# Kernel tuning notes

Hardware: AMD Instinct MI355X
Metric: run time of the kernel (lower is better)

The kernel has to match this reference:

```python
import jax, jax.numpy as jnp
import numpy as np

T = 2048          # tokens
HID = 4096        # hidden_size
H = 32            # n_heads
D = 192           # head_dim
DR = 64           # qk_rope_head_dim
Q_LORA = 1536
O_LORA = 512
G = 4             # o_groups
EPS = 1e-6
MAX_POS = 4096
ROPE_BASE = 10000.0
SCALE = D ** -0.5


def _rmsnorm(x, weight=None, eps=EPS):
    # normalize over last dim in fp32, like the triton kernel / RMSNorm
    xf = x.astype(jnp.float32)
    rms_inv = jax.lax.rsqrt(jnp.mean(xf * xf, axis=-1, keepdims=True) + eps)
    out = xf * rms_inv
    if weight is not None:
        out = out * weight
    return out.astype(x.dtype)


def _apply_rope(x, cos, sin):
    # x: [..., DR]; interleaved complex rotation (deepseek-style freqs_cis mult)
    x2 = x.reshape(x.shape[:-1] + (DR // 2, 2))
    a, b = x2[..., 0], x2[..., 1]
    ra = a * cos - b * sin
    rb = a * sin + b * cos
    return jnp.stack([ra, rb], axis=-1).reshape(x.shape)


def setup_inputs() -> dict:
    key = jax.random.key(0)
    ks = jax.random.split(key, 12)
    s = lambda k, shape, scale: jax.random.normal(k, shape, dtype=jnp.float32) * scale
    x = s(ks[0], (T, HID), 1.0)
    positions = jnp.arange(T, dtype=jnp.int64)
    wq_a = s(ks[1], (Q_LORA, HID), HID ** -0.5)
    q_norm_w = jnp.ones((Q_LORA,), jnp.float32)
    wq_b = s(ks[2], (H * D, Q_LORA), Q_LORA ** -0.5)
    wkv = s(ks[3], (D, HID), HID ** -0.5)
    kv_norm_w = jnp.ones((D,), jnp.float32)
    attn_sink = s(ks[4], (H,), 1.0)
    wo_a = s(ks[5], (G * O_LORA, (H * D) // G), ((H * D) // G) ** -0.5)
    wo_b = s(ks[6], (HID, G * O_LORA), (G * O_LORA) ** -0.5)
    # precomputed rope tables [MAX_POS, DR//2]
    inv_freq = 1.0 / (ROPE_BASE ** (np.arange(0, DR, 2, dtype=np.float32) / DR))
    t = np.arange(MAX_POS, dtype=np.float32)
    freqs = np.outer(t, inv_freq)
    rope_cos = jnp.asarray(np.cos(freqs))
    rope_sin = jnp.asarray(np.sin(freqs))
    return dict(x=x, positions=positions, wq_a=wq_a, q_norm_w=q_norm_w, wq_b=wq_b,
                wkv=wkv, kv_norm_w=kv_norm_w, attn_sink=attn_sink, wo_a=wo_a,
                wo_b=wo_b, rope_cos=rope_cos, rope_sin=rope_sin)


def reference(x, positions, wq_a, q_norm_w, wq_b, wkv, kv_norm_w, attn_sink,
              wo_a, wo_b, rope_cos, rope_sin):
    cos = rope_cos[positions]  # [T, DR//2]
    sin = rope_sin[positions]

    # q path: wq_a -> RMSNorm(weighted) -> wq_b -> per-head unweighted RMSNorm -> RoPE
    q_lora = _rmsnorm(x @ wq_a.T, q_norm_w)                # [T, Q_LORA]
    q = (q_lora @ wq_b.T).reshape(T, H, D)                 # [T, H, D]
    q = _rmsnorm(q)                                        # per-head rms_normalize
    q_rope = _apply_rope(q[..., -DR:], cos[:, None, :], sin[:, None, :])
    q = jnp.concatenate([q[..., :-DR], q_rope], axis=-1)

    # shared single kv head: wkv -> kv_norm -> RoPE on rope dims
    kv = _rmsnorm(x @ wkv.T, kv_norm_w)                    # [T, D]
    kv_rope = _apply_rope(kv[..., -DR:], cos, sin)
    kv = jnp.concatenate([kv[..., :-DR], kv_rope], axis=-1)

    # MQA attention with attention sink and causal mask
    scores = jnp.einsum('thd,sd->ths', q, kv).astype(jnp.float32) * SCALE  # [T,H,S]
    causal = positions[:, None] >= positions[None, :]       # [T, S]
    scores = jnp.where(causal[:, None, :], scores, -jnp.inf)
    sink = jnp.broadcast_to(attn_sink[None, :, None], (T, H, 1))
    logits = jnp.concatenate([scores, sink], axis=-1)       # [T, H, S+1]
    probs = jax.nn.softmax(logits, axis=-1)[..., :-1]       # drop sink column
    out = jnp.einsum('ths,sd->thd', probs.astype(kv.dtype), kv)  # [T, H, D]

    # grouped low-rank output projection: wo_a per group, then wo_b
    out_g = out.reshape(T, G, (H * D) // G)
    wo_a_g = wo_a.reshape(G, O_LORA, (H * D) // G)
    o_low = jnp.einsum('tgi,goi->tgo', out_g, wo_a_g).reshape(T, G * O_LORA)
    y = o_low @ wo_b.T                                      # [T, HID]
    return y
```

## Files before the change

### kernel.cpp

```cpp
#include <hip/hip_runtime.h>
#include <hip/hip_bf16.h>

#define T_TOK 2048
#define HIDN  4096
#define NH    32
#define HD    192
#define QLORA 1536
#define OLORA 512
#define NG    4
#define NFUSE 1728

typedef unsigned short u16;
typedef __attribute__((ext_vector_type(8))) short short8;
typedef __attribute__((ext_vector_type(4))) short short4v;
typedef __attribute__((ext_vector_type(4))) float f32x4;

__device__ __forceinline__ float b2f(u16 u) {
  union { unsigned int u; float f; } x; x.u = ((unsigned int)u) << 16; return x.f;
}
__device__ __forceinline__ u16 f2b(float f) {
  union { float f; unsigned int u; } x; x.f = f;
  unsigned int r = x.u + 0x7fff + ((x.u >> 16) & 1);
  return (u16)(r >> 16);
}

#define GLOAD16(gp, lp) __builtin_amdgcn_global_load_lds( \
    (const __attribute__((address_space(1))) unsigned int*)(gp), \
    (__attribute__((address_space(3))) unsigned int*)(lp), 16, 0, 0)
#define SCHEDB() __builtin_amdgcn_sched_barrier(0)
#define SBAR()   __builtin_amdgcn_s_barrier()

__global__ __launch_bounds__(256) void cast_f32_bf16(const float* __restrict__ src,
                                                     u16* __restrict__ dst, long n4) {
  long i = (long)blockIdx.x * blockDim.x + threadIdx.x;
  long stride = (long)gridDim.x * blockDim.x;
  for (long j = i; j < n4; j += stride) {
    float4 v = *reinterpret_cast<const float4*>(src + j * 4);
    short4v o;
    o[0] = (short)f2b(v.x); o[1] = (short)f2b(v.y);
    o[2] = (short)f2b(v.z); o[3] = (short)f2b(v.w);
    *reinterpret_cast<short4v*>(dst + j * 4) = o;
  }
}

template <int OM>
__global__ __launch_bounds__(256)
void gemm_bt(const u16* __restrict__ A, const u16* __restrict__ B,
             void* __restrict__ Cout, int M, int N, int K,
             int lda, int ldb, int ldc,
             long a_goff, long b_goff, long c_goff) {
  A += (long)blockIdx.z * a_goff;
  B += (long)blockIdx.z * b_goff;
  __shared__ u16 As[2][128 * 32];
  __shared__ u16 Bs[2][128 * 32];
  const int tid = threadIdx.x;
  const int lane = tid & 63;
  const int wave = tid >> 6;
  const int lg = lane >> 4, lr = lane & 15;
  const int wm = (wave >> 1) * 64, wn = (wave & 1) * 64;
  const int m0 = blockIdx.x * 128, n0 = blockIdx.y * 128;

  const int i0 = tid, i1 = tid + 256;
  const int ra0 = i0 >> 2, ka0 = (i0 & 3) * 8;
  const int ra1 = i1 >> 2, ka1 = (i1 & 3) * 8;
  const u16* pA0 = A + (long)(m0 + ra0) * lda + ka0;
  const u16* pA1 = A + (long)(m0 + ra1) * lda + ka1;
  int rb0 = n0 + ra0; if (rb0 > N - 1) rb0 = N - 1;
  int rb1 = n0 + ra1; if (rb1 > N - 1) rb1 = N - 1;
  const u16* pB0 = B + (long)rb0 * ldb + ka0;
  const u16* pB1 = B + (long)rb1 * ldb + ka1;
  const int woff = wave * 1024;

  f32x4 acc[4][4];
#pragma unroll
  for (int a = 0; a < 4; a++)
#pragma unroll
    for (int b = 0; b < 4; b++) acc[a][b] = f32x4{0.f, 0.f, 0.f, 0.f};

  GLOAD16(pA0, (char*)As + woff);
  GLOAD16(pA1, (char*)As + 4096 + woff);
  GLOAD16(pB0, (char*)Bs + woff);
  GLOAD16(pB1, (char*)Bs + 4096 + woff);

  const int nk = K >> 5;
  int buf = 0;
  for (int kk = 0; kk < nk; ++kk) {
    const int kn = (kk + 1 < nk) ? (kk + 1) * 32 : kk * 32;
    {
      char* dA = (char*)As + (buf ^ 1) * 8192 + woff;
      char* dB = (char*)Bs + (buf ^ 1) * 8192 + woff;
      GLOAD16(pA0 + kn, dA);
      GLOAD16(pA1 + kn, dA + 4096);
      GLOAD16(pB0 + kn, dB);
      GLOAD16(pB1 + kn, dB + 4096);
    }
    asm volatile("s_waitcnt vmcnt(4)" ::: "memory");
    SCHEDB(); SBAR(); SCHEDB();

    short8 af[4], bf[4];
#pragma unroll
    for (int i = 0; i < 4; i++)
      af[i] = *reinterpret_cast<const short8*>(&As[buf][(wm + i * 16 + lr) * 32 + lg * 8]);
#pragma unroll
    for (int i = 0; i < 4; i++)
      bf[i] = *reinterpret_cast<const short8*>(&Bs[buf][(wn + i * 16 + lr) * 32 + lg * 8]);
#pragma unroll
    for (int mi = 0; mi < 4; mi++)
#pragma unroll
      for (int ni = 0; ni < 4; ni++)
        acc[mi][ni] = __builtin_amdgcn_mfma_f32_16x16x32_bf16(af[mi], bf[ni], acc[mi][ni], 0, 0, 0);

    SCHEDB(); SBAR(); SCHEDB();
    buf ^= 1;
  }
  asm volatile("s_waitcnt vmcnt(0)" ::: "memory");

  const long cbase = (long)blockIdx.z * c_goff;
#pragma unroll
  for (int mi = 0; mi < 4; mi++) {
#pragma unroll
    for (int ni = 0; ni < 4; ni++) {
      int col = n0 + wn + ni * 16 + lr;
      if (col < N) {
#pragma unroll
        for (int i = 0; i < 4; i++) {
          int row = m0 + wm + mi * 16 + lg * 4 + i;
          float v = acc[mi][ni][i];
          if constexpr (OM == 0)
            reinterpret_cast<u16*>(Cout)[cbase + (long)row * ldc + col] = f2b(v);
          else
            reinterpret_cast<float*>(Cout)[cbase + (long)row * ldc + col] = v;
        }
      }
    }
  }
}

__global__ __launch_bounds__(256)
void rmsnorm_rows(u16* __restrict__ buf, const float* __restrict__ w) {
  const int row = blockIdx.x;
  u16* p = buf + (long)row * NFUSE;
  const int tid = threadIdx.x;
  float v[6];
  float ss = 0.f;
#pragma unroll
  for (int j = 0; j < 6; j++) { v[j] = b2f(p[tid + j * 256]); ss += v[j] * v[j]; }
#pragma unroll
  for (int m = 1; m < 64; m <<= 1) ss += __shfl_xor(ss, m);
  __shared__ float red[4];
  if ((tid & 63) == 0) red[tid >> 6] = ss;
  __syncthreads();
  ss = red[0] + red[1] + red[2] + red[3];
  float rinv = rsqrtf(ss * (1.0f / QLORA) + 1e-6f);
#pragma unroll
  for (int j = 0; j < 6; j++) p[tid + j * 256] = f2b(v[j] * rinv * w[tid + j * 256]);
}

__global__ __launch_bounds__(256)
void qnorm_rope(u16* __restrict__ q, const int* __restrict__ pos,
                const float* __restrict__ rc, const float* __restrict__ rs) {
  const int t = blockIdx.x, h = blockIdx.y * 4 + (threadIdx.x >> 6);
  u16* p = q + (long)t * (NH * HD) + h * HD;
  const int lane = threadIdx.x & 63;
  float v0 = b2f(p[lane]), v1 = b2f(p[lane + 64]), v2 = b2f(p[lane + 128]);
  float ss = v0 * v0 + v1 * v1 + v2 * v2;
#pragma unroll
  for (int m = 1; m < 64; m <<= 1) ss += __shfl_xor(ss, m);
  float rinv = rsqrtf(ss * (1.0f / HD) + 1e-6f);
  v0 *= rinv; v1 *= rinv; v2 *= rinv;
  float partner = __shfl_xor(v2, 1);
  int pp = pos[t];
  int j = lane >> 1;
  float c = rc[pp * 32 + j], s = rs[pp * 32 + j];
  float r = ((lane & 1) == 0) ? (v2 * c - partner * s) : (partner * s + v2 * c);
  p[lane] = f2b(v0); p[lane + 64] = f2b(v1); p[lane + 128] = f2b(r);
}

__global__ __launch_bounds__(256)
void kvnorm_rope(const u16* __restrict__ t1f, u16* __restrict__ kvb,
                 u16* __restrict__ kvT, const float* __restrict__ w,
                 const int* __restrict__ pos,
                 const float* __restrict__ rc, const float* __restrict__ rs) {
  const int t = blockIdx.x * 4 + (threadIdx.x >> 6);
  const u16* src = t1f + (long)t * NFUSE + QLORA;
  u16* p = kvb + (long)t * HD;
  const int lane = threadIdx.x & 63;
  float v0 = b2f(src[lane]), v1 = b2f(src[lane + 64]), v2 = b2f(src[lane + 128]);
  float ss = v0 * v0 + v1 * v1 + v2 * v2;
#pragma unroll
  for (int m = 1; m < 64; m <<= 1) ss += __shfl_xor(ss, m);
  float rinv = rsqrtf(ss * (1.0f / HD) + 1e-6f);
  v0 *= rinv * w[lane]; v1 *= rinv * w[lane + 64]; v2 *= rinv * w[lane + 128];
  float partner = __shfl_xor(v2, 1);
  int pp = pos[t];
  int j = lane >> 1;
  float c = rc[pp * 32 + j], s = rs[pp * 32 + j];
  float r = ((lane & 1) == 0) ? (v2 * c - partner * s) : (partner * s + v2 * c);
  u16 o0 = f2b(v0), o1 = f2b(v1), o2 = f2b(r);
  p[lane] = o0; p[lane + 64] = o1; p[lane + 128] = o2;
  kvT[(long)lane * T_TOK + t] = o0;
  kvT[(long)(lane + 64) * T_TOK + t] = o1;
  kvT[(long)(lane + 128) * T_TOK + t] = o2;
}

__global__ __launch_bounds__(512)
void attn(const u16* __restrict__ q, const u16* __restrict__ kv,
          const u16* __restrict__ kvT, const float* __restrict__ sink,
          u16* __restrict__ out) {
  __shared__ u16 Ks[2][64 * 192];
  __shared__ u16 Vs[2][192 * 64];
  __shared__ u16 P[8][16 * 68];
  const int tid = threadIdx.x;
  const int wave = tid >> 6, lane = tid & 63;
  const int lg = lane >> 4, lr = lane & 15;
  const int h = blockIdx.y * 8 + wave;
  u16* Pw = P[wave];

  int krow[3], koff[3], vrow[3], voff[3];
#pragma unroll
  for (int j = 0; j < 3; j++) {
    int s = tid + j * 512;
    int rk = s / 24, ck = s - rk * 24;
    krow[j] = rk; koff[j] = (ck ^ (rk & 7)) * 8;
    int rv = s >> 3, cv = s & 7;
    vrow[j] = rv; voff[j] = (cv ^ (rv & 7)) * 8;
  }
  const float sk = sink[h];
  const float scale = 0.07216878364870323f;
  int buf = 0;

  for (int pass = 0; pass < 2; ++pass) {
    const int qb = pass ? blockIdx.x : (127 - blockIdx.x);
    const int q0 = qb * 16;
    const int s_end = q0 + 16;
    const int nt = (s_end + 63) >> 6;

    short8 qf[6];
#pragma unroll
    for (int c = 0; c < 6; c++)
      qf[c] = *reinterpret_cast<const short8*>(
          q + (long)(q0 + lr) * (NH * HD) + h * HD + c * 32 + lg * 8);

    f32x4 acc[12];
#pragma unroll
    for (int c = 0; c < 12; c++) acc[c] = f32x4{0.f, 0.f, 0.f, 0.f};
    float mr[4], lrow[4];
#pragma unroll
    for (int i = 0; i < 4; i++) { mr[i] = sk; lrow[i] = 1.0f; }

    {
      char* dK = (char*)Ks[buf]; char* dV = (char*)Vs[buf];
#pragma unroll
      for (int j = 0; j < 3; j++)
        GLOAD16(kv + (long)krow[j] * HD + koff[j], dK + (tid + j * 512) * 16);
#pragma unroll
      for (int j = 0; j < 3; j++)
        GLOAD16(kvT + (long)vrow[j] * T_TOK + voff[j], dV + (tid + j * 512) * 16);
    }

    for (int t = 0; t < nt; ++t) {
      const int s0 = t * 64;
      const int sn = (t + 1 < nt) ? s0 + 64 : s0;
      {
        char* dK = (char*)Ks[buf ^ 1]; char* dV = (char*)Vs[buf ^ 1];
#pragma unroll
        for (int j = 0; j < 3; j++)
          GLOAD16(kv + (long)(sn + krow[j]) * HD + koff[j], dK + (tid + j * 512) * 16);
#pragma unroll
        for (int j = 0; j < 3; j++)
          GLOAD16(kvT + (long)vrow[j] * T_TOK + sn + voff[j], dV + (tid + j * 512) * 16);
      }
      asm volatile("s_waitcnt vmcnt(6)" ::: "memory");
      SCHEDB(); SBAR(); SCHEDB();

      const u16* Kb = Ks[buf];
      const u16* Vb = Vs[buf];
      f32x4 sc[4];
      __builtin_amdgcn_s_setprio(1);
#pragma unroll
      for (int sub = 0; sub < 4; sub++) {
        int c0 = s0 + sub * 16;
        f32x4 v = f32x4{0.f, 0.f, 0.f, 0.f};
        if (c0 < s_end) {
#pragma unroll
          for (int c = 0; c < 6; c++) {
            short8 kf = *reinterpret_cast<const short8*>(
                &Kb[((sub * 16 + lr) * HD + c * 32 + lg * 8) ^ ((lr & 7) << 3)]);
            v = __builtin_amdgcn_mfma_f32_16x16x32_bf16(qf[c], kf, v, 0, 0, 0);
          }
          int scol = c0 + lr;
#pragma unroll
          for (int i = 0; i < 4; i++) {
            int qrow = q0 + lg * 4 + i;
            v[i] = (scol <= qrow) ? v[i] * scale : -__builtin_inff();
          }
        } else {
#pragma unroll
          for (int i = 0; i < 4; i++) v[i] = -__builtin_inff();
        }
        sc[sub] = v;
      }
      __builtin_amdgcn_s_setprio(0);

      float mn[4];
#pragma unroll
      for (int i = 0; i < 4; i++) {
        float tm = fmaxf(fmaxf(sc[0][i], sc[1][i]), fmaxf(sc[2][i], sc[3][i]));
#pragma unroll
        for (int m = 1; m < 16; m <<= 1) tm = fmaxf(tm, __shfl_xor(tm, m));
        mn[i] = fmaxf(mr[i], tm);
      }
      bool need = (mn[0] > mr[0]) | (mn[1] > mr[1]) | (mn[2] > mr[2]) | (mn[3] > mr[3]);
      if (__any(need)) {
#pragma unroll
        for (int i = 0; i < 4; i++) {
          float f = __expf(mr[i] - mn[i]);
          lrow[i] *= f; mr[i] = mn[i];
#pragma unroll
          for (int c = 0; c < 12; c++) acc[c][i] *= f;
        }
      }
      float pr[4][4];
#pragma unroll
      for (int i = 0; i < 4; i++) {
        float rsum = 0.f;
#pragma unroll
        for (int sub = 0; sub < 4; sub++) { pr[sub][i] = __expf(sc[sub][i] - mr[i]); rsum += pr[sub][i]; }
#pragma unroll
        for (int m = 1; m < 16; m <<= 1) rsum += __shfl_xor(rsum, m);
        lrow[i] += rsum;
      }
#pragma unroll
      for (int sub = 0; sub < 4; sub++)
#pragma unroll
        for (int i = 0; i < 4; i++)
          Pw[(lg * 4 + i) * 68 + sub * 16 + lr] = f2b(pr[sub][i]);
      short8 pf0 = *reinterpret_cast<const short8*>(&Pw[lr * 68 + lg * 8]);
      short8 pf1 = *reinterpret_cast<const short8*>(&Pw[lr * 68 + 32 + lg * 8]);

      __builtin_amdgcn_s_setprio(1);
#pragma unroll
      for (int c = 0; c < 12; c++) {
        short8 vf = *reinterpret_cast<const short8*>(
            &Vb[((c * 16 + lr) * 64 + lg * 8) ^ ((lr & 7) << 3)]);
        acc[c] = __builtin_amdgcn_mfma_f32_16x16x32_bf16(pf0, vf, acc[c], 0, 0, 0);
      }
      if (s0 + 32 < s_end) {
#pragma unroll
        for (int c = 0; c < 12; c++) {
          short8 vf = *reinterpret_cast<const short8*>(
              &Vb[((c * 16 + lr) * 64 + 32 + lg * 8) ^ ((lr & 7) << 3)]);
          acc[c] = __builtin_amdgcn_mfma_f32_16x16x32_bf16(pf1, vf, acc[c], 0, 0, 0);
        }
      }
      __builtin_amdgcn_s_setprio(0);

      SCHEDB(); SBAR(); SCHEDB();
      buf ^= 1;
    }

    asm volatile("s_waitcnt vmcnt(0)" ::: "memory");
#pragma unroll
    for (int c = 0; c < 12; c++)
#pragma unroll
      for (int i = 0; i < 4; i++) {
        int qrow = q0 + lg * 4 + i;
        out[(long)qrow * (NH * HD) + h * HD + c * 16 + lr] = f2b(acc[c][i] / lrow[i]);
      }
    SBAR();
  }
}

extern "C" void kernel_launch(void* const* d_in, const int* in_sizes, int n_in,
                              void* d_out, int out_size, void* d_ws, size_t ws_size,
                              hipStream_t stream) {
  const float* x    = (const float*)d_in[0];
  const int* pos    = (const int*)d_in[1];
  const float* wq_a = (const float*)d_in[2];
  const float* q_nw = (const float*)d_in[3];
  const float* wq_b = (const float*)d_in[4];
  const float* wkv  = (const float*)d_in[5];
  const float* kvnw = (const float*)d_in[6];
  const float* sink = (const float*)d_in[7];
  const float* wo_a = (const float*)d_in[8];
  const float* wo_b = (const float*)d_in[9];
  const float* rcos = (const float*)d_in[10];
  const float* rsin = (const float*)d_in[11];
  float* y = (float*)d_out;

  char* ws = (char*)d_ws;
  size_t off = 0;
  auto alloc = [&](size_t bytes) -> void* {
    void* p = ws + off;
    off += (bytes + 255) & ~(size_t)255;
    return p;
  };
  u16* xb   = (u16*)alloc((size_t)T_TOK * HIDN * 2);
  u16* wqab = (u16*)alloc((size_t)QLORA * HIDN * 2);
  u16* wkvb = (u16*)alloc((size_t)HD * HIDN * 2);
  u16* wqbb = (u16*)alloc((size_t)NH * HD * QLORA * 2);
  u16* woab = (u16*)alloc((size_t)NG * OLORA * 1536 * 2);
  u16* wobb = (u16*)alloc((size_t)HIDN * NG * OLORA * 2);
  u16* t1f  = (u16*)alloc((size_t)T_TOK * NFUSE * 2);
  u16* qn   = (u16*)alloc((size_t)T_TOK * NH * HD * 2);
  u16* kvb  = (u16*)alloc((size_t)T_TOK * HD * 2);
  u16* kvT  = (u16*)alloc((size_t)HD * T_TOK * 2);
  u16* ao   = (u16*)alloc((size_t)T_TOK * NH * HD * 2);
  u16* olow = (u16*)alloc((size_t)T_TOK * NG * OLORA * 2);

  auto cast = [&](const float* s, u16* d, long n) {
    long n4 = n / 4;
    long blocks = (n4 + 255) / 256;
    if (blocks > 2048) blocks = 2048;
    hipLaunchKernelGGL(cast_f32_bf16, dim3((int)blocks), dim3(256), 0, stream, s, d, n4);
  };
  cast(x, xb, (long)T_TOK * HIDN);
  cast(wq_a, wqab, (long)QLORA * HIDN);
  cast(wkv, wkvb, (long)HD * HIDN);
  cast(wq_b, wqbb, (long)NH * HD * QLORA);
  cast(wo_a, woab, (long)NG * OLORA * 1536);
  cast(wo_b, wobb, (long)HIDN * NG * OLORA);

  hipLaunchKernelGGL((gemm_bt<0>), dim3(16, 14, 1), dim3(256), 0, stream,
                     xb, wqab, (void*)t1f, 2048, NFUSE, 4096, 4096, 4096, NFUSE, 0L, 0L, 0L);
  hipLaunchKernelGGL(rmsnorm_rows, dim3(2048), dim3(256), 0, stream, t1f, q_nw);
  hipLaunchKernelGGL(kvnorm_rope, dim3(512), dim3(256), 0, stream,
                     t1f, kvb, kvT, kvnw, pos, rcos, rsin);
  hipLaunchKernelGGL((gemm_bt<0>), dim3(16, 48, 1), dim3(256), 0, stream,
                     t1f, wqbb, (void*)qn, 2048, 6144, 1536, NFUSE, 1536, 6144, 0L, 0L, 0L);
  hipLaunchKernelGGL(qnorm_rope, dim3(2048, 8), dim3(256), 0, stream, qn, pos, rcos, rsin);
  hipLaunchKernelGGL(attn, dim3(64, 4), dim3(512), 0, stream, qn, kvb, kvT, sink, ao);
  hipLaunchKernelGGL((gemm_bt<0>), dim3(16, 4, 4), dim3(256), 0, stream,
                     ao, woab, (void*)olow, 2048, 512, 1536, 6144, 1536, 2048,
                     1536L, (long)512 * 1536, 512L);
  hipLaunchKernelGGL((gemm_bt<1>), dim3(16, 32, 1), dim3(256), 0, stream,
                     olow, wobb, (void*)y, 2048, 4096, 2048, 2048, 2048, 4096, 0L, 0L, 0L);
}
```

Baseline: 410.3 us.

## Run both causal passes concurrently in 1024-thread attention blocks, fuse casts, fold scale

The attention kernel now launches 16 waves per block: half handle the long (reversed) query tile and half the short tile, sharing one K/V staging pipeline instead of doing two sequential passes. The softmax scale and log2(e) are folded into Q during qnorm_rope so the kernel can use exp2f and skip the per-score multiply. The six f32->bf16 cast launches are merged into a single kernel. In exchange, the short-tile waves sit idle once their causal range is done, and 1024-thread blocks limit occupancy and register budget.

```diff
diff --git a/kernel.cpp b/kernel.cpp
--- a/kernel.cpp
+++ b/kernel.cpp
@@ -30,17 +30,30 @@
 #define SCHEDB() __builtin_amdgcn_sched_barrier(0)
 #define SBAR()   __builtin_amdgcn_s_barrier()
 
-__global__ __launch_bounds__(256) void cast_f32_bf16(const float* __restrict__ src,
-                                                     u16* __restrict__ dst, long n4) {
-  long i = (long)blockIdx.x * blockDim.x + threadIdx.x;
-  long stride = (long)gridDim.x * blockDim.x;
-  for (long j = i; j < n4; j += stride) {
+__device__ __forceinline__ void cast_seg(const float* __restrict__ src,
+                                         u16* __restrict__ dst, long n4,
+                                         long idx, long stride) {
+  for (long j = idx; j < n4; j += stride) {
     float4 v = *reinterpret_cast<const float4*>(src + j * 4);
     short4v o;
     o[0] = (short)f2b(v.x); o[1] = (short)f2b(v.y);
     o[2] = (short)f2b(v.z); o[3] = (short)f2b(v.w);
     *reinterpret_cast<short4v*>(dst + j * 4) = o;
   }
+}
+
+__global__ __launch_bounds__(256)
+void cast6(const float* s0, u16* d0, long n0, const float* s1, u16* d1, long n1,
+           const float* s2, u16* d2, long n2, const float* s3, u16* d3, long n3,
+           const float* s4, u16* d4, long n4c, const float* s5, u16* d5, long n5) {
+  long idx = (long)blockIdx.x * blockDim.x + threadIdx.x;
+  long stride = (long)gridDim.x * blockDim.x;
+  cast_seg(s0, d0, n0, idx, stride);
+  cast_seg(s1, d1, n1, idx, stride);
+  cast_seg(s2, d2, n2, idx, stride);
+  cast_seg(s3, d3, n3, idx, stride);
+  cast_seg(s4, d4, n4c, idx, stride);
+  cast_seg(s5, d5, n5, idx, stride);
 }
 
 template <int OM>
@@ -162,6 +175,7 @@
   const int t = blockIdx.x, h = blockIdx.y * 4 + (threadIdx.x >> 6);
   u16* p = q + (long)t * (NH * HD) + h * HD;
   const int lane = threadIdx.x & 63;
+  const float QS = 0.07216878364870323f * 1.4426950408889634f;
   float v0 = b2f(p[lane]), v1 = b2f(p[lane + 64]), v2 = b2f(p[lane + 128]);
   float ss = v0 * v0 + v1 * v1 + v2 * v2;
 #pragma unroll
@@ -173,7 +187,7 @@
   int j = lane >> 1;
   float c = rc[pp * 32 + j], s = rs[pp * 32 + j];
   float r = ((lane & 1) == 0) ? (v2 * c - partner * s) : (partner * s + v2 * c);
-  p[lane] = f2b(v0); p[lane + 64] = f2b(v1); p[lane + 128] = f2b(r);
+  p[lane] = f2b(v0 * QS); p[lane + 64] = f2b(v1 * QS); p[lane + 128] = f2b(r * QS);
 }
 
 __global__ __launch_bounds__(256)
@@ -203,76 +217,74 @@
   kvT[(long)(lane + 128) * T_TOK + t] = o2;
 }
 
-__global__ __launch_bounds__(512)
+__global__ __launch_bounds__(1024, 4)
 void attn(const u16* __restrict__ q, const u16* __restrict__ kv,
           const u16* __restrict__ kvT, const float* __restrict__ sink,
           u16* __restrict__ out) {
   __shared__ u16 Ks[2][64 * 192];
   __shared__ u16 Vs[2][192 * 64];
-  __shared__ u16 P[8][16 * 68];
+  __shared__ u16 P[16][16 * 68];
   const int tid = threadIdx.x;
   const int wave = tid >> 6, lane = tid & 63;
   const int lg = lane >> 4, lr = lane & 15;
-  const int h = blockIdx.y * 8 + wave;
+  const int role = wave >> 3;
+  const int h = blockIdx.y * 8 + (wave & 7);
+  const int bx = blockIdx.x;
+  const int q0 = role ? bx * 16 : (127 - bx) * 16;
+  const int s_end = q0 + 16;
+  const int ntL = ((127 - bx) * 16 + 16 + 63) >> 6;
   u16* Pw = P[wave];
 
-  int krow[3], koff[3], vrow[3], voff[3];
+  int srow[3], soff[3], sdst[3], skind[3];
 #pragma unroll
   for (int j = 0; j < 3; j++) {
-    int s = tid + j * 512;
-    int rk = s / 24, ck = s - rk * 24;
-    krow[j] = rk; koff[j] = (ck ^ (rk & 7)) * 8;
-    int rv = s >> 3, cv = s & 7;
-    vrow[j] = rv; voff[j] = (cv ^ (rv & 7)) * 8;
+    int g = j * 1024 + tid;
+    if (g < 1536) {
+      int rk = g / 24, ck = g - rk * 24;
+      srow[j] = rk; soff[j] = (ck ^ (rk & 7)) * 8; sdst[j] = g * 16; skind[j] = 1;
+    } else {
+      int vc = g - 1536;
+      int rv = vc >> 3, cv = vc & 7;
+      srow[j] = rv; soff[j] = (cv ^ (rv & 7)) * 8; sdst[j] = vc * 16; skind[j] = 0;
+    }
   }
-  const float sk = sink[h];
-  const float scale = 0.07216878364870323f;
+
+#define STAGE(BUF, S0) do { \
+    _Pragma("unroll") \
+    for (int j = 0; j < 3; j++) { \
+      if (skind[j]) \
+        GLOAD16(kv + (long)((S0) + srow[j]) * HD + soff[j], (char*)Ks[BUF] + sdst[j]); \
+      else \
+        GLOAD16(kvT + (long)srow[j] * T_TOK + (S0) + soff[j], (char*)Vs[BUF] + sdst[j]); \
+    } \
+  } while (0)
+
+  const float sk = sink[h] * 1.4426950408889634f;
+
+  short8 qf[6];
+#pragma unroll
+  for (int c = 0; c < 6; c++)
+    qf[c] = *reinterpret_cast<const short8*>(
+        q + (long)(q0 + lr) * (NH * HD) + h * HD + c * 32 + lg * 8);
+
+  f32x4 acc[12];
+#pragma unroll
+  for (int c = 0; c < 12; c++) acc[c] = f32x4{0.f, 0.f, 0.f, 0.f};
+  float mr[4], lrow[4];
+#pragma unroll
+  for (int i = 0; i < 4; i++) { mr[i] = sk; lrow[i] = 1.0f; }
+
+  STAGE(0, 0);
+
   int buf = 0;
-
-  for (int pass = 0; pass < 2; ++pass) {
-    const int qb = pass ? blockIdx.x : (127 - blockIdx.x);
-    const int q0 = qb * 16;
-    const int s_end = q0 + 16;
-    const int nt = (s_end + 63) >> 6;
-
-    short8 qf[6];
-#pragma unroll
-    for (int c = 0; c < 6; c++)
-      qf[c] = *reinterpret_cast<const short8*>(
-          q + (long)(q0 + lr) * (NH * HD) + h * HD + c * 32 + lg * 8);
-
-    f32x4 acc[12];
-#pragma unroll
-    for (int c = 0; c < 12; c++) acc[c] = f32x4{0.f, 0.f, 0.f, 0.f};
-    float mr[4], lrow[4];
-#pragma unroll
-    for (int i = 0; i < 4; i++) { mr[i] = sk; lrow[i] = 1.0f; }
-
-    {
-      char* dK = (char*)Ks[buf]; char* dV = (char*)Vs[buf];
-#pragma unroll
-      for (int j = 0; j < 3; j++)
-        GLOAD16(kv + (long)krow[j] * HD + koff[j], dK + (tid + j * 512) * 16);
-#pragma unroll
-      for (int j = 0; j < 3; j++)
-        GLOAD16(kvT + (long)vrow[j] * T_TOK + voff[j], dV + (tid + j * 512) * 16);
-    }
-
-    for (int t = 0; t < nt; ++t) {
-      const int s0 = t * 64;
-      const int sn = (t + 1 < nt) ? s0 + 64 : s0;
-      {
-        char* dK = (char*)Ks[buf ^ 1]; char* dV = (char*)Vs[buf ^ 1];
-#pragma unroll
-        for (int j = 0; j < 3; j++)
-          GLOAD16(kv + (long)(sn + krow[j]) * HD + koff[j], dK + (tid + j * 512) * 16);
-#pragma unroll
-        for (int j = 0; j < 3; j++)
-          GLOAD16(kvT + (long)vrow[j] * T_TOK + sn + voff[j], dV + (tid + j * 512) * 16);
-      }
-      asm volatile("s_waitcnt vmcnt(6)" ::: "memory");
-      SCHEDB(); SBAR(); SCHEDB();
-
+  for (int t = 0; t < ntL; ++t) {
+    const int s0 = t * 64;
+    const int sn = (t + 1 < ntL) ? s0 + 64 : s0;
+    STAGE(buf ^ 1, sn);
+    asm volatile("s_waitcnt vmcnt(3)" ::: "memory");
+    SCHEDB(); SBAR(); SCHEDB();
+
+    if (s0 < s_end) {
       const u16* Kb = Ks[buf];
       const u16* Vb = Vs[buf];
       f32x4 sc[4];
@@ -292,7 +304,7 @@
 #pragma unroll
           for (int i = 0; i < 4; i++) {
             int qrow = q0 + lg * 4 + i;
-            v[i] = (scol <= qrow) ? v[i] * scale : -__builtin_inff();
+            v[i] = (scol <= qrow) ? v[i] : -__builtin_inff();
           }
         } else {
 #pragma unroll
@@ -314,7 +326,7 @@
       if (__any(need)) {
 #pragma unroll
         for (int i = 0; i < 4; i++) {
-          float f = __expf(mr[i] - mn[i]);
+          float f = exp2f(mr[i] - mn[i]);
           lrow[i] *= f; mr[i] = mn[i];
 #pragma unroll
           for (int c = 0; c < 12; c++) acc[c][i] *= f;
@@ -325,7 +337,7 @@
       for (int i = 0; i < 4; i++) {
         float rsum = 0.f;
 #pragma unroll
-        for (int sub = 0; sub < 4; sub++) { pr[sub][i] = __expf(sc[sub][i] - mr[i]); rsum += pr[sub][i]; }
+        for (int sub = 0; sub < 4; sub++) { pr[sub][i] = exp2f(sc[sub][i] - mr[i]); rsum += pr[sub][i]; }
 #pragma unroll
         for (int m = 1; m < 16; m <<= 1) rsum += __shfl_xor(rsum, m);
         lrow[i] += rsum;
@@ -354,21 +366,21 @@
         }
       }
       __builtin_amdgcn_s_setprio(0);
-
-      SCHEDB(); SBAR(); SCHEDB();
-      buf ^= 1;
     }
 
-    asm volatile("s_waitcnt vmcnt(0)" ::: "memory");
-#pragma unroll
-    for (int c = 0; c < 12; c++)
-#pragma unroll
-      for (int i = 0; i < 4; i++) {
-        int qrow = q0 + lg * 4 + i;
-        out[(long)qrow * (NH * HD) + h * HD + c * 16 + lr] = f2b(acc[c][i] / lrow[i]);
-      }
-    SBAR();
+    SCHEDB(); SBAR(); SCHEDB();
+    buf ^= 1;
   }
+  asm volatile("s_waitcnt vmcnt(0)" ::: "memory");
+
+#pragma unroll
+  for (int c = 0; c < 12; c++)
+#pragma unroll
+    for (int i = 0; i < 4; i++) {
+      int qrow = q0 + lg * 4 + i;
+      out[(long)qrow * (NH * HD) + h * HD + c * 16 + lr] = f2b(acc[c][i] / lrow[i]);
+    }
+#undef STAGE
 }
 
 extern "C" void kernel_launch(void* const* d_in, const int* in_sizes, int n_in,
@@ -408,18 +420,13 @@
   u16* ao   = (u16*)alloc((size_t)T_TOK * NH * HD * 2);
   u16* olow = (u16*)alloc((size_t)T_TOK * NG * OLORA * 2);
 
-  auto cast = [&](const float* s, u16* d, long n) {
-    long n4 = n / 4;
-    long blocks = (n4 + 255) / 256;
-    if (blocks > 2048) blocks = 2048;
-    hipLaunchKernelGGL(cast_f32_bf16, dim3((int)blocks), dim3(256), 0, stream, s, d, n4);
-  };
-  cast(x, xb, (long)T_TOK * HIDN);
-  cast(wq_a, wqab, (long)QLORA * HIDN);
-  cast(wkv, wkvb, (long)HD * HIDN);
-  cast(wq_b, wqbb, (long)NH * HD * QLORA);
-  cast(wo_a, woab, (long)NG * OLORA * 1536);
-  cast(wo_b, wobb, (long)HIDN * NG * OLORA);
+  hipLaunchKernelGGL(cast6, dim3(1024), dim3(256), 0, stream,
+                     x,    xb,   (long)T_TOK * HIDN / 4,
+                     wq_a, wqab, (long)QLORA * HIDN / 4,
+                     wkv,  wkvb, (long)HD * HIDN / 4,
+                     wq_b, wqbb, (long)NH * HD * QLORA / 4,
+                     wo_a, woab, (long)NG * OLORA * 1536 / 4,
+                     wo_b, wobb, (long)HIDN * NG * OLORA / 4);
 
   hipLaunchKernelGGL((gemm_bt<0>), dim3(16, 14, 1), dim3(256), 0, stream,
                      xb, wqab, (void*)t1f, 2048, NFUSE, 4096, 4096, 4096, NFUSE, 0L, 0L, 0L);
@@ -429,7 +436,7 @@
   hipLaunchKernelGGL((gemm_bt<0>), dim3(16, 48, 1), dim3(256), 0, stream,
                      t1f, wqbb, (void*)qn, 2048, 6144, 1536, NFUSE, 1536, 6144, 0L, 0L, 0L);
   hipLaunchKernelGGL(qnorm_rope, dim3(2048, 8), dim3(256), 0, stream, qn, pos, rcos, rsin);
-  hipLaunchKernelGGL(attn, dim3(64, 4), dim3(512), 0, stream, qn, kvb, kvT, sink, ao);
+  hipLaunchKernelGGL(attn, dim3(64, 4), dim3(1024), 0, stream, qn, kvb, kvT, sink, ao);
   hipLaunchKernelGGL((gemm_bt<0>), dim3(16, 4, 4), dim3(256), 0, stream,
                      ao, woab, (void*)olow, 2048, 512, 1536, 6144, 1536, 2048,
                      1536L, (long)512 * 1536, 512L);
```

After: 723.3 us. 1.76x slower.

## Fuse weight casts, swizzle GEMM block order, fold softmax scale into q

Applied to the files above, without the earlier changes.

The six fp32-to-bf16 cast launches become a single grid-stride kernel. GEMM blocks are remapped with an XCD-style swizzle (groups of 8) to improve L2 locality across chiplets. The attention scale and log2(e) are folded into q during the norm/rope pass so the softmax can use exp2 without a per-score multiply; this rounds the scaled q to bf16, which slightly changes numerics.

```diff
diff --git a/kernel.cpp b/kernel.cpp
--- a/kernel.cpp
+++ b/kernel.cpp
@@ -30,17 +30,30 @@
 #define SCHEDB() __builtin_amdgcn_sched_barrier(0)
 #define SBAR()   __builtin_amdgcn_s_barrier()
 
-__global__ __launch_bounds__(256) void cast_f32_bf16(const float* __restrict__ src,
-                                                     u16* __restrict__ dst, long n4) {
-  long i = (long)blockIdx.x * blockDim.x + threadIdx.x;
-  long stride = (long)gridDim.x * blockDim.x;
-  for (long j = i; j < n4; j += stride) {
+__device__ __forceinline__ void cast_seg(const float* __restrict__ src,
+                                         u16* __restrict__ dst, long n4,
+                                         long idx, long stride) {
+  for (long j = idx; j < n4; j += stride) {
     float4 v = *reinterpret_cast<const float4*>(src + j * 4);
     short4v o;
     o[0] = (short)f2b(v.x); o[1] = (short)f2b(v.y);
     o[2] = (short)f2b(v.z); o[3] = (short)f2b(v.w);
     *reinterpret_cast<short4v*>(dst + j * 4) = o;
   }
+}
+
+__global__ __launch_bounds__(256)
+void cast6(const float* s0, u16* d0, long n0, const float* s1, u16* d1, long n1,
+           const float* s2, u16* d2, long n2, const float* s3, u16* d3, long n3,
+           const float* s4, u16* d4, long n4c, const float* s5, u16* d5, long n5) {
+  long idx = (long)blockIdx.x * blockDim.x + threadIdx.x;
+  long stride = (long)gridDim.x * blockDim.x;
+  cast_seg(s0, d0, n0, idx, stride);
+  cast_seg(s1, d1, n1, idx, stride);
+  cast_seg(s2, d2, n2, idx, stride);
+  cast_seg(s3, d3, n3, idx, stride);
+  cast_seg(s4, d4, n4c, idx, stride);
+  cast_seg(s5, d5, n5, idx, stride);
 }
 
 template <int OM>
@@ -58,7 +71,17 @@
   const int wave = tid >> 6;
   const int lg = lane >> 4, lr = lane & 15;
   const int wm = (wave >> 1) * 64, wn = (wave & 1) * 64;
-  const int m0 = blockIdx.x * 128, n0 = blockIdx.y * 128;
+
+  int bx = blockIdx.x, by = blockIdx.y;
+  {
+    int nx = gridDim.x, nwg = nx * gridDim.y;
+    if ((nwg & 7) == 0) {
+      int lin = by * nx + bx;
+      int swz = (lin & 7) * (nwg >> 3) + (lin >> 3);
+      bx = swz % nx; by = swz / nx;
+    }
+  }
+  const int m0 = bx * 128, n0 = by * 128;
 
   const int i0 = tid, i1 = tid + 256;
   const int ra0 = i0 >> 2, ka0 = (i0 & 3) * 8;
@@ -162,6 +185,7 @@
   const int t = blockIdx.x, h = blockIdx.y * 4 + (threadIdx.x >> 6);
   u16* p = q + (long)t * (NH * HD) + h * HD;
   const int lane = threadIdx.x & 63;
+  const float QS = 0.07216878364870323f * 1.4426950408889634f;
   float v0 = b2f(p[lane]), v1 = b2f(p[lane + 64]), v2 = b2f(p[lane + 128]);
   float ss = v0 * v0 + v1 * v1 + v2 * v2;
 #pragma unroll
@@ -173,7 +197,7 @@
   int j = lane >> 1;
   float c = rc[pp * 32 + j], s = rs[pp * 32 + j];
   float r = ((lane & 1) == 0) ? (v2 * c - partner * s) : (partner * s + v2 * c);
-  p[lane] = f2b(v0); p[lane + 64] = f2b(v1); p[lane + 128] = f2b(r);
+  p[lane] = f2b(v0 * QS); p[lane + 64] = f2b(v1 * QS); p[lane + 128] = f2b(r * QS);
 }
 
 __global__ __launch_bounds__(256)
@@ -225,12 +249,11 @@
     int rv = s >> 3, cv = s & 7;
     vrow[j] = rv; voff[j] = (cv ^ (rv & 7)) * 8;
   }
-  const float sk = sink[h];
-  const float scale = 0.07216878364870323f;
+  const float sk = sink[h] * 1.4426950408889634f;
   int buf = 0;
 
   for (int pass = 0; pass < 2; ++pass) {
-    const int qb = pass ? blockIdx.x : (127 - blockIdx.x);
+    const int qb = pass ? (int)blockIdx.x : (127 - (int)blockIdx.x);
     const int q0 = qb * 16;
     const int s_end = q0 + 16;
     const int nt = (s_end + 63) >> 6;
@@ -292,7 +315,7 @@
 #pragma unroll
           for (int i = 0; i < 4; i++) {
             int qrow = q0 + lg * 4 + i;
-            v[i] = (scol <= qrow) ? v[i] * scale : -__builtin_inff();
+            v[i] = (scol <= qrow) ? v[i] : -__builtin_inff();
           }
         } else {
 #pragma unroll
@@ -314,7 +337,7 @@
       if (__any(need)) {
 #pragma unroll
         for (int i = 0; i < 4; i++) {
-          float f = __expf(mr[i] - mn[i]);
+          float f = exp2f(mr[i] - mn[i]);
           lrow[i] *= f; mr[i] = mn[i];
 #pragma unroll
           for (int c = 0; c < 12; c++) acc[c][i] *= f;
@@ -325,7 +348,7 @@
       for (int i = 0; i < 4; i++) {
         float rsum = 0.f;
 #pragma unroll
-        for (int sub = 0; sub < 4; sub++) { pr[sub][i] = __expf(sc[sub][i] - mr[i]); rsum += pr[sub][i]; }
+        for (int sub = 0; sub < 4; sub++) { pr[sub][i] = exp2f(sc[sub][i] - mr[i]); rsum += pr[sub][i]; }
 #pragma unroll
         for (int m = 1; m < 16; m <<= 1) rsum += __shfl_xor(rsum, m);
         lrow[i] += rsum;
@@ -408,18 +431,13 @@
   u16* ao   = (u16*)alloc((size_t)T_TOK * NH * HD * 2);
   u16* olow = (u16*)alloc((size_t)T_TOK * NG * OLORA * 2);
 
-  auto cast = [&](const float* s, u16* d, long n) {
-    long n4 = n / 4;
-    long blocks = (n4 + 255) / 256;
-    if (blocks > 2048) blocks = 2048;
-    hipLaunchKernelGGL(cast_f32_bf16, dim3((int)blocks), dim3(256), 0, stream, s, d, n4);
-  };
-  cast(x, xb, (long)T_TOK * HIDN);
-  cast(wq_a, wqab, (long)QLORA * HIDN);
-  cast(wkv, wkvb, (long)HD * HIDN);
-  cast(wq_b, wqbb, (long)NH * HD * QLORA);
-  cast(wo_a, woab, (long)NG * OLORA * 1536);
-  cast(wo_b, wobb, (long)HIDN * NG * OLORA);
+  hipLaunchKernelGGL(cast6, dim3(1024), dim3(256), 0, stream,
+                     x,    xb,   (long)T_TOK * HIDN / 4,
+                     wq_a, wqab, (long)QLORA * HIDN / 4,
+                     wkv,  wkvb, (long)HD * HIDN / 4,
+                     wq_b, wqbb, (long)NH * HD * QLORA / 4,
+                     wo_a, woab, (long)NG * OLORA * 1536 / 4,
+                     wo_b, wobb, (long)HIDN * NG * OLORA / 4);
 
   hipLaunchKernelGGL((gemm_bt<0>), dim3(16, 14, 1), dim3(256), 0, stream,
                      xb, wqab, (void*)t1f, 2048, NFUSE, 4096, 4096, 4096, NFUSE, 0L, 0L, 0L);
```

Result: no change. 408.4 us (-0.5%).
